# Optimization experiments

Measured on AMD Instinct MI355X. Metric: run time of the kernel, lower is better.

Reference implementation:

```python
import jax, jax.numpy as jnp
import numpy as np

B, C, D, H, W = 8, 256, 128, 64, 64  # batch, in_channels, inter_dim, spatial
BN_EPS = 1e-5


def setup_inputs() -> dict:
    key = jax.random.key(0)
    ks = jax.random.split(key, 6)
    s_c = 1.0 / np.sqrt(C)
    s_d = 1.0 / np.sqrt(D)
    return {
        "x": jax.random.normal(ks[0], (B, C, H, W), dtype=jnp.float32),
        # 1x1 conv kernels, stored as [out_ch, in_ch]
        "theta_w": jax.random.normal(ks[1], (D, C), dtype=jnp.float32) * s_c,
        "phi_w": jax.random.normal(ks[2], (D, C), dtype=jnp.float32) * s_c,
        "g_w": jax.random.normal(ks[3], (D, C), dtype=jnp.float32) * s_c,
        "w_w": jax.random.normal(ks[4], (C, D), dtype=jnp.float32) * s_d,
        "w_b": jnp.zeros((C,), dtype=jnp.float32),
        "bn_gamma": jnp.ones((C,), dtype=jnp.float32),
        "bn_beta": jnp.zeros((C,), dtype=jnp.float32),
    }


def reference(x, theta_w, phi_w, g_w, w_w, w_b, bn_gamma, bn_beta):
    Bs, Cs, Hs, Ws = x.shape
    N = Hs * Ws
    xf = x.reshape(Bs, Cs, N)  # flatten spatial -> [B, C, N]

    # 1x1 convs (bias=False) == per-position channel matmuls
    theta = jnp.einsum('dc,bcn->bnd', theta_w, xf)  # [B, N, D]
    phi = jnp.einsum('dc,bcn->bdn', phi_w, xf)      # [B, D, N]
    g = jnp.einsum('dc,bcn->bnd', g_w, xf)          # [B, N, D]

    # embedded-Gaussian attention: softmax(theta @ phi) @ g
    f = jnp.einsum('bnd,bdm->bnm', theta, phi)      # [B, N, N]
    f_div_C = jax.nn.softmax(f, axis=-1)
    y = jnp.einsum('bnm,bmd->bnd', f_div_C, g)      # [B, N, D]

    # output projection W (1x1 conv with bias)
    w_y = jnp.einsum('cd,bnd->bcn', w_w, y) + w_b[None, :, None]  # [B, C, N]

    # BatchNorm (training mode: batch statistics, biased variance)
    mean = w_y.mean(axis=(0, 2))
    var = jnp.mean(jnp.square(w_y - mean[None, :, None]), axis=(0, 2))
    scale = (bn_gamma * jax.lax.rsqrt(var + BN_EPS))[None, :, None]
    w_y = (w_y - mean[None, :, None]) * scale + bn_beta[None, :, None]

    z = w_y + xf  # residual
    return z.reshape(Bs, Cs, Hs, Ws)
```

## Files before the change

### kernel.cpp

```cpp
#include <hip/hip_runtime.h>

#define BB 8
#define CC 256
#define DD 128
#define NN 4096
#define BN_EPS 1e-5f

typedef _Float16 f16;
typedef _Float16 half8 __attribute__((ext_vector_type(8)));
typedef _Float16 half2t __attribute__((ext_vector_type(2)));
typedef float f32x4 __attribute__((ext_vector_type(4)));

__device__ __forceinline__ f32x4 mfma16(half8 a, half8 b, f32x4 c) {
  return __builtin_amdgcn_mfma_f32_16x16x32_f16(a, b, c, 0, 0, 0);
}

__device__ __forceinline__ void gload_lds16(const void* g, void* l) {
  __builtin_amdgcn_global_load_lds((const __attribute__((address_space(1))) void*)g,
                                   (__attribute__((address_space(3))) void*)l, 16, 0, 0);
}

__device__ __forceinline__ half2t pkrtz(float a, float b) {
  auto t = __builtin_amdgcn_cvt_pkrtz(a, b);
  return __builtin_bit_cast(half2t, t);
}

#define EXP2(x) __builtin_amdgcn_exp2f(x)

#define PERM32(i) ((((i) >> 2) & 3) * 8 + (((i) >> 4) & 1) * 4 + ((i) & 3))

__global__ void k_cast_weights(const float* __restrict__ tw, const float* __restrict__ pw,
                               const float* __restrict__ gw, const float* __restrict__ ww,
                               f16* __restrict__ Wcat, f16* __restrict__ Wwh,
                               float* __restrict__ stats) {
  int i = blockIdx.x * 256 + threadIdx.x;
  if (i < 32768) Wcat[i] = (f16)tw[i];
  else if (i < 65536) Wcat[i] = (f16)pw[i - 32768];
  else if (i < 98304) Wcat[i] = (f16)gw[i - 65536];
  else if (i < 131072) Wwh[i - 98304] = (f16)ww[i - 98304];
  if (i < 512) stats[i] = 0.f;
}

__global__ __launch_bounds__(256) void k_gemm1(const float* __restrict__ x, const f16* __restrict__ Wcat,
                                               f16* __restrict__ T, f16* __restrict__ P,
                                               f16* __restrict__ Gdn) {
  __shared__ char xls[32768];
  __shared__ char gls[16384];
  int b = blockIdx.y;
  int n0 = blockIdx.x * 64;
  int tid = threadIdx.x;
  int lane = tid & 63, wave = tid >> 6;
  int lr = lane & 15, lg = lane >> 4;
  int wr = wave >> 1, wc = wave & 1;

  {
    int c = tid;
    const float* src = x + ((size_t)b * CC + c) * NN + n0;
#pragma unroll
    for (int n4 = 0; n4 < 64; n4 += 4) {
      f32x4 v = *(const f32x4*)(src + n4);
#pragma unroll
      for (int k = 0; k < 4; ++k) {
        int n = n4 + k;
        *(f16*)(xls + n * 512 + ((((c >> 3) ^ (n & 7)) * 8 + (c & 7)) * 2)) = (f16)v[k];
      }
    }
  }
  __syncthreads();

  half8 a[2][8];
#pragma unroll
  for (int i = 0; i < 2; ++i) {
    int nloc = wr * 32 + i * 16 + lr;
#pragma unroll
    for (int k0 = 0; k0 < 8; ++k0)
      a[i][k0] = *(const half8*)(xls + nloc * 512 + (((k0 * 4 + lg) ^ (nloc & 7)) << 4));
  }

  size_t base = (size_t)b * NN + n0;
#pragma unroll
  for (int yb = 0; yb < 6; ++yb) {
    int c0 = yb * 64 + wc * 32;
    f32x4 acc[2][2] = {};
#pragma unroll
    for (int k0 = 0; k0 < 8; ++k0) {
      half8 w[2];
      for (int j = 0; j < 2; ++j)
        w[j] = *(const half8*)(Wcat + (size_t)(c0 + j * 16 + lr) * CC + k0 * 32 + lg * 8);
      for (int i = 0; i < 2; ++i)
        for (int j = 0; j < 2; ++j)
          acc[i][j] = mfma16(a[i][k0], w[j], acc[i][j]);
    }
    if (yb < 4) {
      f16* dst = (yb < 2) ? T : P;
      int cl0 = (yb & 1) * 64 + wc * 32;
      for (int i = 0; i < 2; ++i)
        for (int j = 0; j < 2; ++j)
          for (int r = 0; r < 4; ++r) {
            int row = wr * 32 + i * 16 + lg * 4 + r;
            int col = cl0 + j * 16 + lr;
            dst[(base + row) * DD + col] = (f16)acc[i][j][r];
          }
    } else {
      for (int i = 0; i < 2; ++i)
        for (int j = 0; j < 2; ++j)
          for (int r = 0; r < 4; ++r) {
            int n = wr * 32 + i * 16 + lg * 4 + r;
            int d = (yb - 4) * 64 + wc * 32 + j * 16 + lr;
            *(f16*)(gls + n * 256 + ((((d >> 3) ^ (n & 7)) * 8 + (d & 7)) * 2)) = (f16)acc[i][j][r];
          }
    }
  }
  __syncthreads();
  {
    int d = tid >> 1, nh = (tid & 1) * 32;
    f16 tmp[32];
#pragma unroll
    for (int k = 0; k < 32; ++k) {
      int n = nh + k;
      tmp[k] = *(const f16*)(gls + n * 256 + ((((d >> 3) ^ (n & 7)) * 8 + (d & 7)) * 2));
    }
    f16* dst = Gdn + ((size_t)b * DD + d) * NN + n0 + nh;
#pragma unroll
    for (int k = 0; k < 4; ++k)
      *(half8*)(dst + k * 8) = *(const half8*)(tmp + k * 8);
  }
}

__global__ __launch_bounds__(256, 3) void k_flash(const f16* __restrict__ T, const f16* __restrict__ P,
                                                  const f16* __restrict__ Gdn, f16* __restrict__ accs,
                                                  float* __restrict__ ml) {
  __shared__ char smem[32768];
  int bid = blockIdx.x;
  int b = bid & 7;
  int u = bid >> 3;
  int hf = u % 3;
  int qx = u / 3;
  int t0 = (hf == 2) ? 86 : hf * 43;
  int nt = (hf == 2) ? 42 : 43;
  int tid = threadIdx.x;
  int lane = tid & 63, wave = tid >> 6;
  int lr = lane & 15, lg = lane >> 4;
  int q0 = qx * 128 + wave * 32;
  const f16* Tb = T + (size_t)b * NN * DD;
  const f16* Pb = P + ((size_t)b * NN + t0 * 32) * DD;
  const f16* Vb = Gdn + (size_t)b * DD * NN + t0 * 32;
  int srcq = 4 * lg;

  const f16* kbase[2];
  const f16* vbase[2];
  char* kdst[2];
  char* vdst[2];
#pragma unroll
  for (int inst = 0; inst < 2; ++inst) {
    int t = inst * 256 + tid;
    int row = t >> 4, sp = t & 15, sl = sp ^ (row & 7);
    kbase[inst] = Pb + (size_t)PERM32(row) * DD + sl * 8;
    kdst[inst] = smem + (inst * 256 + wave * 64) * 16;
    int dv = t >> 2, gv = t & 3, glv = gv ^ ((dv >> 1) & 3);
    vbase[inst] = Vb + (size_t)dv * NN + glv * 8;
    vdst[inst] = smem + 16384 + (inst * 256 + wave * 64) * 16;
  }

  half8 qf[2][4];
  for (int qt = 0; qt < 2; ++qt)
    for (int ks = 0; ks < 4; ++ks) {
      half8 v = *(const half8*)(Tb + (size_t)(q0 + qt * 16 + lr) * DD + ks * 32 + lg * 8);
      for (int j = 0; j < 8; ++j) v[j] *= (f16)1.44269504f;
      qf[qt][ks] = v;
    }
  half8 ones;
  for (int j = 0; j < 8; ++j) ones[j] = (f16)1.f;

  f32x4 acc[2][8] = {};
  f32x4 lsum[2] = {};
  float m_run[2] = {-1e30f, -1e30f};

#pragma unroll
  for (int inst = 0; inst < 2; ++inst) gload_lds16(kbase[inst], kdst[inst]);
#pragma unroll
  for (int inst = 0; inst < 2; ++inst) gload_lds16(vbase[inst], vdst[inst]);

  for (int kb = 0; kb < nt; ++kb) {
    int keyn = (kb < nt - 1) ? kb * 32 + 32 : 0;
    int cur = (kb & 1) * 8192, nxt = ((kb + 1) & 1) * 8192;
    char* Kc = smem + cur;
    char* Vc = smem + 16384 + cur;

    size_t ko = (size_t)keyn * DD;
#pragma unroll
    for (int inst = 0; inst < 2; ++inst) gload_lds16(kbase[inst] + ko, kdst[inst] + nxt);
    asm volatile("s_waitcnt vmcnt(4)" ::: "memory");
    __builtin_amdgcn_sched_barrier(0);
    __builtin_amdgcn_s_barrier();
    __builtin_amdgcn_sched_barrier(0);

    f32x4 s[2][2];
    __builtin_amdgcn_s_setprio(1);
    for (int kt = 0; kt < 2; ++kt) {
      half8 kf[4];
      for (int ks = 0; ks < 4; ++ks)
        kf[ks] = *(const half8*)(Kc + (kt * 16 + lr) * 256 + (((ks * 4 + lg) ^ (lr & 7)) << 4));
      for (int qt = 0; qt < 2; ++qt) {
        f32x4 t = {};
        for (int ks = 0; ks < 4; ++ks) t = mfma16(kf[ks], qf[qt][ks], t);
        s[qt][kt] = t;
      }
    }
    __builtin_amdgcn_s_setprio(0);

    half8 af[2];
    for (int qt = 0; qt < 2; ++qt) {
      float mx = fmaxf(fmaxf(s[qt][0][0], s[qt][0][1]), fmaxf(s[qt][0][2], s[qt][0][3]));
      mx = fmaxf(mx, fmaxf(fmaxf(s[qt][1][0], s[qt][1][1]), fmaxf(s[qt][1][2], s[qt][1][3])));
      mx = fmaxf(mx, __shfl_xor(mx, 16));
      mx = fmaxf(mx, __shfl_xor(mx, 32));
      bool grow = mx > m_run[qt] + 11.5f;
      if (__ballot(grow)) {
        float mn = fmaxf(m_run[qt], mx);
        float corr = EXP2(m_run[qt] - mn);
        m_run[qt] = mn;
        float c0 = __shfl(corr, srcq + 0), c1 = __shfl(corr, srcq + 1);
        float c2 = __shfl(corr, srcq + 2), c3 = __shfl(corr, srcq + 3);
        lsum[qt][0] *= c0; lsum[qt][1] *= c1; lsum[qt][2] *= c2; lsum[qt][3] *= c3;
        for (int nb = 0; nb < 8; ++nb) {
          acc[qt][nb][0] *= c0; acc[qt][nb][1] *= c1;
          acc[qt][nb][2] *= c2; acc[qt][nb][3] *= c3;
        }
      }
      for (int kt = 0; kt < 2; ++kt)
        for (int r = 0; r < 4; ++r)
          s[qt][kt][r] = EXP2(s[qt][kt][r] - m_run[qt]);
      union { half8 h8; half2t h2[4]; } un;
      un.h2[0] = pkrtz(s[qt][0][0], s[qt][0][1]);
      un.h2[1] = pkrtz(s[qt][0][2], s[qt][0][3]);
      un.h2[2] = pkrtz(s[qt][1][0], s[qt][1][1]);
      un.h2[3] = pkrtz(s[qt][1][2], s[qt][1][3]);
      af[qt] = un.h8;
      lsum[qt] = mfma16(af[qt], ones, lsum[qt]);
    }

#pragma unroll
    for (int inst = 0; inst < 2; ++inst) gload_lds16(vbase[inst] + keyn, vdst[inst] + nxt);
    asm volatile("s_waitcnt vmcnt(4)" ::: "memory");
    __builtin_amdgcn_sched_barrier(0);
    __builtin_amdgcn_s_barrier();
    __builtin_amdgcn_sched_barrier(0);

    __builtin_amdgcn_s_setprio(1);
    for (int nb = 0; nb < 8; ++nb) {
      int d = nb * 16 + lr;
      half8 vf = *(const half8*)(Vc + d * 64 + ((lg ^ ((d >> 1) & 3)) << 4));
      acc[0][nb] = mfma16(af[0], vf, acc[0][nb]);
      acc[1][nb] = mfma16(af[1], vf, acc[1][nb]);
    }
    __builtin_amdgcn_s_setprio(0);
  }
  asm volatile("s_waitcnt vmcnt(0)" ::: "memory");

  size_t gq0 = (size_t)b * NN + q0;
  f16* A = accs + (size_t)hf * ((size_t)BB * NN * DD) + gq0 * DD;
  for (int qt = 0; qt < 2; ++qt)
    for (int nb = 0; nb < 8; ++nb)
      for (int r = 0; r < 4; ++r)
        A[(size_t)(qt * 16 + lg * 4 + r) * DD + nb * 16 + lr] = (f16)acc[qt][nb][r];
  float* mArr = ml + hf * 32768;
  float* lArr = ml + 98304 + hf * 32768;
  if (lg == 0) {
    mArr[gq0 + lr] = m_run[0];
    mArr[gq0 + 16 + lr] = m_run[1];
  }
  if (lr == 0)
    for (int r = 0; r < 4; ++r) {
      lArr[gq0 + lg * 4 + r] = lsum[0][r];
      lArr[gq0 + 16 + lg * 4 + r] = lsum[1][r];
    }
}

__global__ void k_merge(f16* __restrict__ accs, const float* __restrict__ ml) {
  int idx = blockIdx.x * 256 + threadIdx.x;
  int q = idx >> 4, dc = (idx & 15) * 8;
  float m0 = ml[q], m1 = ml[32768 + q], m2 = ml[65536 + q];
  float l0 = ml[98304 + q], l1 = ml[131072 + q], l2 = ml[163840 + q];
  float mm = fmaxf(fmaxf(m0, m1), m2);
  float c0 = EXP2(m0 - mm), c1 = EXP2(m1 - mm), c2 = EXP2(m2 - mm);
  float inv = 1.f / (l0 * c0 + l1 * c1 + l2 * c2);
  c0 *= inv; c1 *= inv; c2 *= inv;
  const size_t SEG = (size_t)BB * NN * DD;
  size_t off = (size_t)q * DD + dc;
  half8 v0 = *(const half8*)(accs + off);
  half8 v1 = *(const half8*)(accs + SEG + off);
  half8 v2 = *(const half8*)(accs + 2 * SEG + off);
  half8 o;
  for (int j = 0; j < 8; ++j)
    o[j] = (f16)((float)v0[j] * c0 + (float)v1[j] * c1 + (float)v2[j] * c2);
  *(half8*)(accs + off) = o;
}

__global__ __launch_bounds__(256) void k_gemm2(const f16* __restrict__ Y, const f16* __restrict__ Wwh,
                                               const float* __restrict__ wb, f16* __restrict__ wy,
                                               float* __restrict__ stats) {
  __shared__ float part[2][8][64];
  int lane = threadIdx.x & 63, wave = threadIdx.x >> 6;
  int lr = lane & 15, lg = lane >> 4;
  int wr = wave >> 1, wc = wave & 1;
  int c0 = blockIdx.y * 64 + wc * 32;
  half8 w[4][2];
  for (int k0 = 0; k0 < 4; ++k0)
    for (int j = 0; j < 2; ++j)
      w[k0][j] = *(const half8*)(Wwh + (size_t)(c0 + j * 16 + lr) * DD + k0 * 32 + lg * 8);
  float bias[2];
  for (int j = 0; j < 2; ++j) bias[j] = wb[c0 + j * 16 + lr];
  float ps[2][2] = {};
  for (int mt = 0; mt < 8; ++mt) {
    int m0 = (blockIdx.x * 8 + mt) * 64 + wr * 32;
    f32x4 acc[2][2] = {};
    for (int k0 = 0; k0 < 4; ++k0) {
      half8 a[2];
      for (int i = 0; i < 2; ++i)
        a[i] = *(const half8*)(Y + (size_t)(m0 + i * 16 + lr) * DD + k0 * 32 + lg * 8);
      for (int i = 0; i < 2; ++i)
        for (int j = 0; j < 2; ++j)
          acc[i][j] = mfma16(a[i], w[k0][j], acc[i][j]);
    }
    for (int i = 0; i < 2; ++i)
      for (int j = 0; j < 2; ++j)
        for (int r = 0; r < 4; ++r) {
          int row = m0 + i * 16 + lg * 4 + r;
          int col = c0 + j * 16 + lr;
          float v = acc[i][j][r] + bias[j];
          wy[(size_t)row * CC + col] = (f16)v;
          ps[j][0] += v;
          ps[j][1] += v * v;
        }
  }
  for (int j = 0; j < 2; ++j) {
    int colL = wc * 32 + j * 16 + lr;
    part[0][wr * 4 + lg][colL] = ps[j][0];
    part[1][wr * 4 + lg][colL] = ps[j][1];
  }
  __syncthreads();
  if (threadIdx.x < 128) {
    int metric = threadIdx.x >> 6, col = threadIdx.x & 63;
    float s = 0.f;
    for (int wtr = 0; wtr < 8; ++wtr) s += part[metric][wtr][col];
    atomicAdd(&stats[metric * CC + blockIdx.y * 64 + col], s);
  }
}

__global__ void k_bn_apply(const f16* __restrict__ wy, const float* __restrict__ x,
                           const float* __restrict__ stats, const float* __restrict__ gamma,
                           const float* __restrict__ beta, float* __restrict__ out) {
  __shared__ f16 tile[32][33];
  int b = blockIdx.z, c0 = blockIdx.y * 32, n0 = blockIdx.x * 32;
  int tx = threadIdx.x, ty = threadIdx.y;
  for (int j = 0; j < 4; ++j) {
    int nn = ty + j * 8;
    tile[nn][tx] = wy[((size_t)b * NN + n0 + nn) * CC + c0 + tx];
  }
  __syncthreads();
  const float inv_cnt = 1.f / (float)(BB * NN);
  for (int j = 0; j < 4; ++j) {
    int cc = ty + j * 8;
    int c = c0 + cc;
    float mean = stats[c] * inv_cnt;
    float var = stats[CC + c] * inv_cnt - mean * mean;
    float scale = gamma[c] * rsqrtf(var + BN_EPS);
    size_t oi = ((size_t)b * CC + c) * NN + n0 + tx;
    out[oi] = ((float)tile[tx][cc] - mean) * scale + beta[c] + x[oi];
  }
}

extern "C" void kernel_launch(void* const* d_in, const int* in_sizes, int n_in,
                              void* d_out, int out_size, void* d_ws, size_t ws_size,
                              hipStream_t stream) {
  const float* x = (const float*)d_in[0];
  const float* tw = (const float*)d_in[1];
  const float* pw = (const float*)d_in[2];
  const float* gw = (const float*)d_in[3];
  const float* ww = (const float*)d_in[4];
  const float* wb = (const float*)d_in[5];
  const float* gamma = (const float*)d_in[6];
  const float* beta = (const float*)d_in[7];
  float* out = (float*)d_out;
  char* ws = (char*)d_ws;

  f16* Wcat = (f16*)(ws + 0);
  f16* Wwh = (f16*)(ws + 196608);
  float* stats = (float*)(ws + 262144);
  float* ml = (float*)(ws + 524288);
  const size_t BASE = 1 << 22;
  f16* T = (f16*)(ws + BASE);
  f16* P = (f16*)(ws + BASE + 8388608);
  f16* Gdn = (f16*)(ws + BASE + 16777216);
  f16* accs = (f16*)(ws + BASE + 25165824);
  f16* wy = (f16*)(ws + BASE);

  k_cast_weights<<<512, 256, 0, stream>>>(tw, pw, gw, ww, Wcat, Wwh, stats);
  k_gemm1<<<dim3(NN / 64, BB), 256, 0, stream>>>(x, Wcat, T, P, Gdn);
  k_flash<<<768, 256, 0, stream>>>(T, P, Gdn, accs, ml);
  k_merge<<<2048, 256, 0, stream>>>(accs, ml);
  k_gemm2<<<dim3(BB * NN / 512, CC / 64), 256, 0, stream>>>(accs, Wwh, wb, wy, stats);
  k_bn_apply<<<dim3(NN / 32, CC / 32, BB), dim3(32, 8), 0, stream>>>(wy, x, stats, gamma, beta, out);
}
```

Baseline: 161.6 us.

## Load flash-attention K fragments directly into registers instead of staging through LDS

Each wave now reads its K (phi) MFMA fragments straight from global memory into registers, prefetching the next key tile during the softmax and PV phase. This drops the K double buffer from shared memory, halving LDS use, and removes one block-wide barrier per key iteration. The vmcnt waits are reordered so the V global-to-LDS copy is issued after the PV MFMAs. In exchange, the four waves of a block now fetch the same K tile from global memory separately (relying on cache hits), and the kernel holds more registers for the prefetched fragments.

Result: slower. 226.1 us (+39.9%).

```diff
diff --git a/kernel.cpp b/kernel.cpp
--- a/kernel.cpp
+++ b/kernel.cpp
@@ -130,7 +130,7 @@
 __global__ __launch_bounds__(256, 3) void k_flash(const f16* __restrict__ T, const f16* __restrict__ P,
                                                   const f16* __restrict__ Gdn, f16* __restrict__ accs,
                                                   float* __restrict__ ml) {
-  __shared__ char smem[32768];
+  __shared__ char smem[16384];
   int bid = blockIdx.x;
   int b = bid & 7;
   int u = bid >> 3;
@@ -147,19 +147,19 @@
   const f16* Vb = Gdn + (size_t)b * DD * NN + t0 * 32;
   int srcq = 4 * lg;
 
-  const f16* kbase[2];
+  const f16* kfb[2];
+#pragma unroll
+  for (int kt = 0; kt < 2; ++kt)
+    kfb[kt] = Pb + (size_t)PERM32(kt * 16 + lr) * DD + lg * 8;
+
   const f16* vbase[2];
-  char* kdst[2];
   char* vdst[2];
 #pragma unroll
   for (int inst = 0; inst < 2; ++inst) {
     int t = inst * 256 + tid;
-    int row = t >> 4, sp = t & 15, sl = sp ^ (row & 7);
-    kbase[inst] = Pb + (size_t)PERM32(row) * DD + sl * 8;
-    kdst[inst] = smem + (inst * 256 + wave * 64) * 16;
     int dv = t >> 2, gv = t & 3, glv = gv ^ ((dv >> 1) & 3);
     vbase[inst] = Vb + (size_t)dv * NN + glv * 8;
-    vdst[inst] = smem + 16384 + (inst * 256 + wave * 64) * 16;
+    vdst[inst] = smem + (inst * 256 + wave * 64) * 16;
   }
 
   half8 qf[2][4];
@@ -176,37 +176,31 @@
   f32x4 lsum[2] = {};
   float m_run[2] = {-1e30f, -1e30f};
 
-#pragma unroll
-  for (int inst = 0; inst < 2; ++inst) gload_lds16(kbase[inst], kdst[inst]);
+  half8 kf[2][4];
+#pragma unroll
+  for (int kt = 0; kt < 2; ++kt)
+#pragma unroll
+    for (int ks = 0; ks < 4; ++ks)
+      kf[kt][ks] = *(const half8*)(kfb[kt] + ks * 32);
 #pragma unroll
   for (int inst = 0; inst < 2; ++inst) gload_lds16(vbase[inst], vdst[inst]);
 
   for (int kb = 0; kb < nt; ++kb) {
     int keyn = (kb < nt - 1) ? kb * 32 + 32 : 0;
     int cur = (kb & 1) * 8192, nxt = ((kb + 1) & 1) * 8192;
-    char* Kc = smem + cur;
-    char* Vc = smem + 16384 + cur;
-
-    size_t ko = (size_t)keyn * DD;
-#pragma unroll
-    for (int inst = 0; inst < 2; ++inst) gload_lds16(kbase[inst] + ko, kdst[inst] + nxt);
-    asm volatile("s_waitcnt vmcnt(4)" ::: "memory");
-    __builtin_amdgcn_sched_barrier(0);
-    __builtin_amdgcn_s_barrier();
+    char* Vc = smem + cur;
+
+    asm volatile("s_waitcnt vmcnt(2)" ::: "memory");
     __builtin_amdgcn_sched_barrier(0);
 
     f32x4 s[2][2];
     __builtin_amdgcn_s_setprio(1);
-    for (int kt = 0; kt < 2; ++kt) {
-      half8 kf[4];
-      for (int ks = 0; ks < 4; ++ks)
-        kf[ks] = *(const half8*)(Kc + (kt * 16 + lr) * 256 + (((ks * 4 + lg) ^ (lr & 7)) << 4));
+    for (int kt = 0; kt < 2; ++kt)
       for (int qt = 0; qt < 2; ++qt) {
         f32x4 t = {};
-        for (int ks = 0; ks < 4; ++ks) t = mfma16(kf[ks], qf[qt][ks], t);
+        for (int ks = 0; ks < 4; ++ks) t = mfma16(kf[kt][ks], qf[qt][ks], t);
         s[qt][kt] = t;
       }
-    }
     __builtin_amdgcn_s_setprio(0);
 
     half8 af[2];
@@ -240,9 +234,16 @@
       lsum[qt] = mfma16(af[qt], ones, lsum[qt]);
     }
 
-#pragma unroll
-    for (int inst = 0; inst < 2; ++inst) gload_lds16(vbase[inst] + keyn, vdst[inst] + nxt);
-    asm volatile("s_waitcnt vmcnt(4)" ::: "memory");
+    {
+      size_t ko = (size_t)keyn * DD;
+#pragma unroll
+      for (int kt = 0; kt < 2; ++kt)
+#pragma unroll
+        for (int ks = 0; ks < 4; ++ks)
+          kf[kt][ks] = *(const half8*)(kfb[kt] + ko + ks * 32);
+    }
+
+    asm volatile("s_waitcnt vmcnt(8)" ::: "memory");
     __builtin_amdgcn_sched_barrier(0);
     __builtin_amdgcn_s_barrier();
     __builtin_amdgcn_sched_barrier(0);
@@ -255,6 +256,9 @@
       acc[1][nb] = mfma16(af[1], vf, acc[1][nb]);
     }
     __builtin_amdgcn_s_setprio(0);
+
+#pragma unroll
+    for (int inst = 0; inst < 2; ++inst) gload_lds16(vbase[inst] + keyn, vdst[inst] + nxt);
   }
   asm volatile("s_waitcnt vmcnt(0)" ::: "memory");
 
```
